# Optimization experiments

Hardware: AMD Instinct MI355X
Metric: run time of the kernel (lower is better)

Reference implementation:

```python
import jax, jax.numpy as jnp
import numpy as np
from jax import lax

N_QUBITS = 8
DEPTH = 2
IN_DIM = 512
LN_EPS = 1e-5


def _ry_shared(state, w, theta_w):
    # RY(theta) on wire w, shared angle across the batch. state: [B, 2,...,2]
    ax = w + 1
    c = jnp.cos(theta_w / 2)
    s = jnp.sin(theta_w / 2)
    s0 = lax.index_in_dim(state, 0, axis=ax, keepdims=True)
    s1 = lax.index_in_dim(state, 1, axis=ax, keepdims=True)
    return jnp.concatenate([c * s0 - s * s1, s * s0 + c * s1], axis=ax)


def _cnot(state, cw, tw):
    # CNOT control=cw, target=tw. state: [B, 2,...,2]
    ax_c = cw + 1
    ax_t = tw + 1
    s0 = lax.index_in_dim(state, 0, axis=ax_c, keepdims=True)
    s1 = lax.index_in_dim(state, 1, axis=ax_c, keepdims=True)
    s1 = jnp.flip(s1, axis=ax_t)
    return jnp.concatenate([s0, s1], axis=ax_c)


def _circuit(angles, theta):
    # angles: [B, n]; theta: [n]. Batched statevector sim (RY/CNOT are real).
    B, n = angles.shape
    half = angles * 0.5
    c = jnp.cos(half)
    s = jnp.sin(half)
    # Initial RY layer on |0...0> is a product state: qubit i -> [cos, sin]
    state = jnp.ones((B,), dtype=angles.dtype)
    for i in range(n):
        amp = jnp.stack([c[:, i], s[:, i]], axis=-1)  # [B, 2]
        state = state[..., None] * amp.reshape((B,) + (1,) * i + (2,))
    # state: [B, 2, 2, ..., 2] (n qubit axes)
    for _ in range(DEPTH):
        for i in range(n):
            state = _cnot(state, i, (i + 1) % n)
        for i in range(n):
            state = _ry_shared(state, i, theta[i])
    # <Z_i> = P(bit_i=0) - P(bit_i=1)
    p = state * state
    zs = []
    for i in range(n):
        axes = tuple(a for a in range(1, n + 1) if a != i + 1)
        m = p.sum(axis=axes)  # [B, 2]
        zs.append(m[:, 0] - m[:, 1])
    return jnp.stack(zs, axis=-1)  # [B, n]


def setup_inputs() -> dict:
    key = jax.random.key(0)
    ks = jax.random.split(key, 6)
    B = 131072
    return {
        "E": jax.random.normal(ks[0], (B, IN_DIM), dtype=jnp.float32),
        "ln_gamma": jnp.ones((IN_DIM,), dtype=jnp.float32),
        "ln_beta": jnp.zeros((IN_DIM,), dtype=jnp.float32),
        "W_pre": jax.random.normal(ks[1], (N_QUBITS, IN_DIM), dtype=jnp.float32) * (1.0 / np.sqrt(IN_DIM)),
        "b_pre": jax.random.normal(ks[2], (N_QUBITS,), dtype=jnp.float32) * 0.02,
        "theta": jax.random.normal(ks[3], (N_QUBITS,), dtype=jnp.float32) * 0.1,
        "W_post": jax.random.normal(ks[4], (1, N_QUBITS), dtype=jnp.float32) * (1.0 / np.sqrt(N_QUBITS)),
        "b_post": jax.random.normal(ks[5], (1,), dtype=jnp.float32) * 0.02,
    }


def reference(E, ln_gamma, ln_beta, W_pre, b_pre, theta, W_post, b_post):
    # pre: LayerNorm + Linear(in_dim -> n_qubits)
    mu = E.mean(axis=-1, keepdims=True)
    var = ((E - mu) ** 2).mean(axis=-1, keepdims=True)
    x = (E - mu) * lax.rsqrt(var + LN_EPS) * ln_gamma + ln_beta
    angles = x @ W_pre.T + b_pre  # [B, n_qubits]
    Z = _circuit(angles, theta)  # [B, n_qubits]
    logit_known = (Z @ W_post.T + b_post)[:, 0]  # squeeze(-1)
    return logit_known
```

## Files before the change

### kernel.cpp

```cpp
#include <hip/hip_runtime.h>

#define BLOCK 256
#define WPW   16

__device__ __forceinline__ float rfl(float x) {
  return __uint_as_float(__builtin_amdgcn_readfirstlane(__float_as_uint(x)));
}

template<int CTRL>
__device__ __forceinline__ float dppmov(float x) {
  return __int_as_float(__builtin_amdgcn_update_dpp(
      0, __float_as_int(x), CTRL, 0xf, 0xf, true));
}
__device__ __forceinline__ float dx1(float x) { return dppmov<0xB1>(x); }
__device__ __forceinline__ float dx2(float x) { return dppmov<0x4E>(x); }
__device__ __forceinline__ float dx4(float x) {
  return dppmov<0x1B>(dppmov<0x141>(x));
}
__device__ __forceinline__ float dx8(float x) { return dppmov<0x128>(x); }
__device__ __forceinline__ float sx16(float x) { return __shfl_xor(x, 16, 64); }
__device__ __forceinline__ float sx32(float x) { return __shfl_xor(x, 32, 64); }

template<int M>
__device__ __forceinline__ float lxor(float x) {
  if constexpr (M == 1)  return dx1(x);
  else if constexpr (M == 2)  return dx2(x);
  else if constexpr (M == 4)  return dx4(x);
  else if constexpr (M == 8)  return dx8(x);
  else if constexpr (M == 16) return sx16(x);
  else                        return sx32(x);
}

__device__ __forceinline__ float wave_allsum(float x) {
  x += dx1(x); x += dx2(x); x += dx4(x); x += dx8(x);
  x += sx16(x); x += sx32(x);
  return x;
}

__global__ __launch_bounds__(BLOCK, 4) void qsco_kernel(
    const float* __restrict__ E,
    const float* __restrict__ ln_gamma,
    const float* __restrict__ ln_beta,
    const float* __restrict__ Wpre,
    const float* __restrict__ bpre,
    const float* __restrict__ theta,
    const float* __restrict__ Wpost,
    const float* __restrict__ bpost,
    float* __restrict__ out,
    int nrows)
{
  const int lane = threadIdx.x & 63;
  const int wave = blockIdx.x * (BLOCK / 64) + (threadIdx.x >> 6);
  const int row0 = wave * WPW;
  if (row0 >= nrows) return;
  const int rowEnd = min(row0 + WPW, nrows);

  const int kA = lane << 2;
  const int kB = 256 + (lane << 2);

  const float4 gamA = *(const float4*)(ln_gamma + kA);
  const float4 gamB = *(const float4*)(ln_gamma + kB);
  const float4 betA = *(const float4*)(ln_beta + kA);
  const float4 betB = *(const float4*)(ln_beta + kB);

  float4 gv[8][2];
  float G[8], K[8];
#pragma unroll
  for (int j = 0; j < 8; ++j) {
    const float4 wA = *(const float4*)(Wpre + j * 512 + kA);
    const float4 wB = *(const float4*)(Wpre + j * 512 + kB);
    float4 ga, gb;
    ga.x = wA.x * gamA.x; ga.y = wA.y * gamA.y; ga.z = wA.z * gamA.z; ga.w = wA.w * gamA.w;
    gb.x = wB.x * gamB.x; gb.y = wB.y * gamB.y; gb.z = wB.z * gamB.z; gb.w = wB.w * gamB.w;
    gv[j][0] = ga; gv[j][1] = gb;
    float gs = (ga.x + ga.y + ga.z + ga.w) + (gb.x + gb.y + gb.z + gb.w);
    float ks = wA.x * betA.x + wA.y * betA.y + wA.z * betA.z + wA.w * betA.w
             + wB.x * betB.x + wB.y * betB.y + wB.z * betB.z + wB.w * betB.w;
    G[j] = rfl(wave_allsum(gs));
    K[j] = rfl(wave_allsum(ks) + bpre[j]);
  }

  float cT[8], sT[8];
#pragma unroll
  for (int q = 0; q < 8; ++q) {
    const float h = 0.5f * theta[q];
    cT[q] = rfl(__cosf(h));
    sT[q] = rfl(__sinf(h));
  }
  float ss[6];
#pragma unroll
  for (int q = 2; q < 8; ++q)
    ss[q - 2] = ((lane >> (q - 2)) & 1) ? sT[q] : -sT[q];

  float al[8];
#pragma unroll
  for (int q = 0; q < 8; ++q) al[q] = rfl(Wpost[q]);
  float base = 0.f;
#pragma unroll
  for (int q = 2; q < 8; ++q)
    base += ((lane >> (q - 2)) & 1) ? -al[q] : al[q];
  const float D0 = base + al[0] + al[1];
  const float D1 = base - al[0] + al[1];
  const float D2 = base + al[0] - al[1];
  const float D3 = base - al[0] - al[1];
  const float bp = rfl(bpost[0]);

  const float* Ep = E + (size_t)row0 * 512;
  float4 eA = *(const float4*)(Ep + kA);
  float4 eB = *(const float4*)(Ep + kB);

  for (int r = row0; r < rowEnd; ++r) {
    float4 nA = eA, nB = eB;
    if (r + 1 < rowEnd) {
      const float* En = E + (size_t)(r + 1) * 512;
      nA = *(const float4*)(En + kA);
      nB = *(const float4*)(En + kB);
    }

    float f[10];
    f[0] = (eA.x + eA.y + eA.z + eA.w) + (eB.x + eB.y + eB.z + eB.w);
    f[1] = eA.x * eA.x + eA.y * eA.y + eA.z * eA.z + eA.w * eA.w
         + eB.x * eB.x + eB.y * eB.y + eB.z * eB.z + eB.w * eB.w;
#pragma unroll
    for (int j = 0; j < 8; ++j) {
      const float4 ga = gv[j][0], gb = gv[j][1];
      f[2 + j] = eA.x * ga.x + eA.y * ga.y + eA.z * ga.z + eA.w * ga.w
               + eB.x * gb.x + eB.y * gb.y + eB.z * gb.z + eB.w * gb.w;
    }
#pragma unroll
    for (int i = 0; i < 10; ++i) f[i] += dx1(f[i]);
#pragma unroll
    for (int i = 0; i < 10; ++i) f[i] += dx2(f[i]);
#pragma unroll
    for (int i = 0; i < 10; ++i) f[i] += dx4(f[i]);
#pragma unroll
    for (int i = 0; i < 10; ++i) f[i] += dx8(f[i]);
#pragma unroll
    for (int i = 0; i < 10; ++i) f[i] += sx16(f[i]);
#pragma unroll
    for (int i = 0; i < 10; ++i) f[i] += sx32(f[i]);

    const float mu = f[0] * (1.0f / 512.0f);
    const float var = f[1] * (1.0f / 512.0f) - mu * mu;
    const float rstd = rsqrtf(var + 1e-5f);

    float ca[8], sa[8];
#pragma unroll
    for (int j = 0; j < 8; ++j) {
      const float ang = rstd * (f[2 + j] - mu * G[j]) + K[j];
      const float h = 0.5f * ang;
      ca[j] = __cosf(h);
      sa[j] = __sinf(h);
    }

    float p = ((lane & 1)  ? sa[2] : ca[2]);
    p      *= ((lane & 2)  ? sa[3] : ca[3]);
    p      *= ((lane & 4)  ? sa[4] : ca[4]);
    p      *= ((lane & 8)  ? sa[5] : ca[5]);
    p      *= ((lane & 16) ? sa[6] : ca[6]);
    p      *= ((lane & 32) ? sa[7] : ca[7]);
    const float pc = p * ca[1], ps = p * sa[1];
    float a0 = pc * ca[0], a1 = pc * sa[0], a2 = ps * ca[0], a3 = ps * sa[0];

#define CNOT_STEP(TM, CM) { \
      const float v0 = lxor<TM>(a0); \
      const float v1 = lxor<TM>(a1); \
      const float v2 = lxor<TM>(a2); \
      const float v3 = lxor<TM>(a3); \
      const bool c = (lane & (CM)) != 0; \
      a0 = c ? v0 : a0; a1 = c ? v1 : a1; a2 = c ? v2 : a2; a3 = c ? v3 : a3; }

#define RY_STEP(M, I) { \
      const float p0 = lxor<M>(a0); \
      const float p1 = lxor<M>(a1); \
      const float p2 = lxor<M>(a2); \
      const float p3 = lxor<M>(a3); \
      a0 = cT[(I) + 2] * a0 + ss[I] * p0; \
      a1 = cT[(I) + 2] * a1 + ss[I] * p1; \
      a2 = cT[(I) + 2] * a2 + ss[I] * p2; \
      a3 = cT[(I) + 2] * a3 + ss[I] * p3; }

#pragma unroll
    for (int d = 0; d < 2; ++d) {
      { const float t = a1; a1 = a3; a3 = t; }
      a2 = dx1(a2);
      a3 = dx1(a3);
      CNOT_STEP(2, 1)
      CNOT_STEP(4, 2)
      CNOT_STEP(8, 4)
      CNOT_STEP(16, 8)
      CNOT_STEP(32, 16)
      { const bool c = (lane & 32) != 0;
        const float t0 = c ? a1 : a0, t1 = c ? a0 : a1;
        const float t2 = c ? a3 : a2, t3 = c ? a2 : a3;
        a0 = t0; a1 = t1; a2 = t2; a3 = t3; }
      { float t = a0; a0 = cT[0] * t - sT[0] * a1; a1 = sT[0] * t + cT[0] * a1;
        t = a2;       a2 = cT[0] * t - sT[0] * a3; a3 = sT[0] * t + cT[0] * a3; }
      { float t = a0; a0 = cT[1] * t - sT[1] * a2; a2 = sT[1] * t + cT[1] * a2;
        t = a1;       a1 = cT[1] * t - sT[1] * a3; a3 = sT[1] * t + cT[1] * a3; }
      RY_STEP(1, 0)
      RY_STEP(2, 1)
      RY_STEP(4, 2)
      RY_STEP(8, 3)
      RY_STEP(16, 4)
      RY_STEP(32, 5)
    }
#undef CNOT_STEP
#undef RY_STEP

    float v = (a0 * a0) * D0 + (a1 * a1) * D1 + (a2 * a2) * D2 + (a3 * a3) * D3;
    v = wave_allsum(v);
    if (lane == 0) out[r] = v + bp;

    eA = nA; eB = nB;
  }
}

extern "C" void kernel_launch(void* const* d_in, const int* in_sizes, int n_in,
                              void* d_out, int out_size, void* d_ws, size_t ws_size,
                              hipStream_t stream) {
  const float* E        = (const float*)d_in[0];
  const float* ln_gamma = (const float*)d_in[1];
  const float* ln_beta  = (const float*)d_in[2];
  const float* Wpre     = (const float*)d_in[3];
  const float* bpre     = (const float*)d_in[4];
  const float* theta    = (const float*)d_in[5];
  const float* Wpost    = (const float*)d_in[6];
  const float* bpost    = (const float*)d_in[7];
  float* out = (float*)d_out;

  const int nrows = in_sizes[0] / 512;
  const int rows_per_block = (BLOCK / 64) * WPW;
  const int grid = (nrows + rows_per_block - 1) / rows_per_block;
  qsco_kernel<<<grid, BLOCK, 0, stream>>>(E, ln_gamma, ln_beta, Wpre, bpre,
                                          theta, Wpost, bpost, out, nrows);
}
```

Measured before the change: 397.2 us.

## Map 16 rows per wave with 4 lanes per row and register-held statevector

Result: slower. 405.5 us (+2.1%).

```diff
diff --git a/kernel.cpp b/kernel.cpp
--- a/kernel.cpp
+++ b/kernel.cpp
@@ -1,7 +1,6 @@
 #include <hip/hip_runtime.h>
 
 #define BLOCK 256
-#define WPW   16
 
 __device__ __forceinline__ float rfl(float x) {
   return __uint_as_float(__builtin_amdgcn_readfirstlane(__float_as_uint(x)));
@@ -21,21 +20,12 @@
 __device__ __forceinline__ float sx16(float x) { return __shfl_xor(x, 16, 64); }
 __device__ __forceinline__ float sx32(float x) { return __shfl_xor(x, 32, 64); }
 
-template<int M>
-__device__ __forceinline__ float lxor(float x) {
-  if constexpr (M == 1)  return dx1(x);
-  else if constexpr (M == 2)  return dx2(x);
-  else if constexpr (M == 4)  return dx4(x);
-  else if constexpr (M == 8)  return dx8(x);
-  else if constexpr (M == 16) return sx16(x);
-  else                        return sx32(x);
-}
-
 __device__ __forceinline__ float wave_allsum(float x) {
   x += dx1(x); x += dx2(x); x += dx4(x); x += dx8(x);
   x += sx16(x); x += sx32(x);
   return x;
 }
+
 
 __global__ __launch_bounds__(BLOCK, 4) void qsco_kernel(
     const float* __restrict__ E,
@@ -49,33 +39,37 @@
     float* __restrict__ out,
     int nrows)
 {
-  const int lane = threadIdx.x & 63;
-  const int wave = blockIdx.x * (BLOCK / 64) + (threadIdx.x >> 6);
-  const int row0 = wave * WPW;
-  if (row0 >= nrows) return;
-  const int rowEnd = min(row0 + WPW, nrows);
-
-  const int kA = lane << 2;
-  const int kB = 256 + (lane << 2);
-
-  const float4 gamA = *(const float4*)(ln_gamma + kA);
-  const float4 gamB = *(const float4*)(ln_gamma + kB);
-  const float4 betA = *(const float4*)(ln_beta + kA);
-  const float4 betB = *(const float4*)(ln_beta + kB);
-
-  float4 gv[8][2];
+  __shared__ float Wg[8][512];
+
+  const int tid  = threadIdx.x;
+  const int lane = tid & 63;
+
+#pragma unroll
+  for (int t = 0; t < 4; ++t) {
+    const int e4 = (t * BLOCK + tid) << 2;
+    const int j = e4 >> 9, k = e4 & 511;
+    const float4 w = *(const float4*)(Wpre + j * 512 + k);
+    const float4 g = *(const float4*)(ln_gamma + k);
+    float4 r;
+    r.x = w.x * g.x; r.y = w.y * g.y; r.z = w.z * g.z; r.w = w.w * g.w;
+    *(float4*)(&Wg[j][k]) = r;
+  }
+  __syncthreads();
+
+  const int k0 = lane << 3;
+  const float4 gamA = *(const float4*)(ln_gamma + k0);
+  const float4 gamB = *(const float4*)(ln_gamma + k0 + 4);
+  const float4 betA = *(const float4*)(ln_beta + k0);
+  const float4 betB = *(const float4*)(ln_beta + k0 + 4);
   float G[8], K[8];
 #pragma unroll
   for (int j = 0; j < 8; ++j) {
-    const float4 wA = *(const float4*)(Wpre + j * 512 + kA);
-    const float4 wB = *(const float4*)(Wpre + j * 512 + kB);
-    float4 ga, gb;
-    ga.x = wA.x * gamA.x; ga.y = wA.y * gamA.y; ga.z = wA.z * gamA.z; ga.w = wA.w * gamA.w;
-    gb.x = wB.x * gamB.x; gb.y = wB.y * gamB.y; gb.z = wB.z * gamB.z; gb.w = wB.w * gamB.w;
-    gv[j][0] = ga; gv[j][1] = gb;
-    float gs = (ga.x + ga.y + ga.z + ga.w) + (gb.x + gb.y + gb.z + gb.w);
-    float ks = wA.x * betA.x + wA.y * betA.y + wA.z * betA.z + wA.w * betA.w
-             + wB.x * betB.x + wB.y * betB.y + wB.z * betB.z + wB.w * betB.w;
+    const float4 wA = *(const float4*)(Wpre + j * 512 + k0);
+    const float4 wB = *(const float4*)(Wpre + j * 512 + k0 + 4);
+    const float gs = wA.x*gamA.x + wA.y*gamA.y + wA.z*gamA.z + wA.w*gamA.w
+                   + wB.x*gamB.x + wB.y*gamB.y + wB.z*gamB.z + wB.w*gamB.w;
+    const float ks = wA.x*betA.x + wA.y*betA.y + wA.z*betA.z + wA.w*betA.w
+                   + wB.x*betB.x + wB.y*betB.y + wB.z*betB.z + wB.w*betB.w;
     G[j] = rfl(wave_allsum(gs));
     K[j] = rfl(wave_allsum(ks) + bpre[j]);
   }
@@ -87,133 +81,154 @@
     cT[q] = rfl(__cosf(h));
     sT[q] = rfl(__sinf(h));
   }
-  float ss[6];
-#pragma unroll
-  for (int q = 2; q < 8; ++q)
-    ss[q - 2] = ((lane >> (q - 2)) & 1) ? sT[q] : -sT[q];
+  const float ss6 = (lane & 1) ? sT[6] : -sT[6];
+  const float ss7 = (lane & 2) ? sT[7] : -sT[7];
 
   float al[8];
 #pragma unroll
   for (int q = 0; q < 8; ++q) al[q] = rfl(Wpost[q]);
-  float base = 0.f;
-#pragma unroll
-  for (int q = 2; q < 8; ++q)
-    base += ((lane >> (q - 2)) & 1) ? -al[q] : al[q];
-  const float D0 = base + al[0] + al[1];
-  const float D1 = base - al[0] + al[1];
-  const float D2 = base + al[0] - al[1];
-  const float D3 = base - al[0] - al[1];
+  const float lsign = ((lane & 1) ? -al[6] : al[6]) + ((lane & 2) ? -al[7] : al[7]);
   const float bp = rfl(bpost[0]);
 
-  const float* Ep = E + (size_t)row0 * 512;
-  float4 eA = *(const float4*)(Ep + kA);
-  float4 eB = *(const float4*)(Ep + kB);
-
-  for (int r = row0; r < rowEnd; ++r) {
-    float4 nA = eA, nB = eB;
-    if (r + 1 < rowEnd) {
-      const float* En = E + (size_t)(r + 1) * 512;
-      nA = *(const float4*)(En + kA);
-      nB = *(const float4*)(En + kB);
-    }
-
-    float f[10];
-    f[0] = (eA.x + eA.y + eA.z + eA.w) + (eB.x + eB.y + eB.z + eB.w);
-    f[1] = eA.x * eA.x + eA.y * eA.y + eA.z * eA.z + eA.w * eA.w
-         + eB.x * eB.x + eB.y * eB.y + eB.z * eB.z + eB.w * eB.w;
+  const int wave = blockIdx.x * (BLOCK / 64) + (tid >> 6);
+  const int row  = wave * 16 + (lane >> 2);
+  const int sub  = lane & 3;
+  const float* Erow = E + (size_t)(row < nrows ? row : 0) * 512 + (sub << 2);
+
+  float f[10];
+#pragma unroll
+  for (int t = 0; t < 10; ++t) f[t] = 0.f;
+#pragma unroll 4
+  for (int i = 0; i < 32; ++i) {
+    const float4 ev = *(const float4*)(Erow + (i << 4));
+    const int kk = (sub << 2) + (i << 4);
+    f[0] += (ev.x + ev.y) + (ev.z + ev.w);
+    f[1] += ev.x*ev.x + ev.y*ev.y + ev.z*ev.z + ev.w*ev.w;
 #pragma unroll
     for (int j = 0; j < 8; ++j) {
-      const float4 ga = gv[j][0], gb = gv[j][1];
-      f[2 + j] = eA.x * ga.x + eA.y * ga.y + eA.z * ga.z + eA.w * ga.w
-               + eB.x * gb.x + eB.y * gb.y + eB.z * gb.z + eB.w * gb.w;
-    }
-#pragma unroll
-    for (int i = 0; i < 10; ++i) f[i] += dx1(f[i]);
-#pragma unroll
-    for (int i = 0; i < 10; ++i) f[i] += dx2(f[i]);
-#pragma unroll
-    for (int i = 0; i < 10; ++i) f[i] += dx4(f[i]);
-#pragma unroll
-    for (int i = 0; i < 10; ++i) f[i] += dx8(f[i]);
-#pragma unroll
-    for (int i = 0; i < 10; ++i) f[i] += sx16(f[i]);
-#pragma unroll
-    for (int i = 0; i < 10; ++i) f[i] += sx32(f[i]);
-
-    const float mu = f[0] * (1.0f / 512.0f);
-    const float var = f[1] * (1.0f / 512.0f) - mu * mu;
-    const float rstd = rsqrtf(var + 1e-5f);
-
-    float ca[8], sa[8];
-#pragma unroll
-    for (int j = 0; j < 8; ++j) {
-      const float ang = rstd * (f[2 + j] - mu * G[j]) + K[j];
-      const float h = 0.5f * ang;
-      ca[j] = __cosf(h);
-      sa[j] = __sinf(h);
-    }
-
-    float p = ((lane & 1)  ? sa[2] : ca[2]);
-    p      *= ((lane & 2)  ? sa[3] : ca[3]);
-    p      *= ((lane & 4)  ? sa[4] : ca[4]);
-    p      *= ((lane & 8)  ? sa[5] : ca[5]);
-    p      *= ((lane & 16) ? sa[6] : ca[6]);
-    p      *= ((lane & 32) ? sa[7] : ca[7]);
-    const float pc = p * ca[1], ps = p * sa[1];
-    float a0 = pc * ca[0], a1 = pc * sa[0], a2 = ps * ca[0], a3 = ps * sa[0];
-
-#define CNOT_STEP(TM, CM) { \
-      const float v0 = lxor<TM>(a0); \
-      const float v1 = lxor<TM>(a1); \
-      const float v2 = lxor<TM>(a2); \
-      const float v3 = lxor<TM>(a3); \
-      const bool c = (lane & (CM)) != 0; \
-      a0 = c ? v0 : a0; a1 = c ? v1 : a1; a2 = c ? v2 : a2; a3 = c ? v3 : a3; }
-
-#define RY_STEP(M, I) { \
-      const float p0 = lxor<M>(a0); \
-      const float p1 = lxor<M>(a1); \
-      const float p2 = lxor<M>(a2); \
-      const float p3 = lxor<M>(a3); \
-      a0 = cT[(I) + 2] * a0 + ss[I] * p0; \
-      a1 = cT[(I) + 2] * a1 + ss[I] * p1; \
-      a2 = cT[(I) + 2] * a2 + ss[I] * p2; \
-      a3 = cT[(I) + 2] * a3 + ss[I] * p3; }
-
-#pragma unroll
-    for (int d = 0; d < 2; ++d) {
-      { const float t = a1; a1 = a3; a3 = t; }
-      a2 = dx1(a2);
-      a3 = dx1(a3);
-      CNOT_STEP(2, 1)
-      CNOT_STEP(4, 2)
-      CNOT_STEP(8, 4)
-      CNOT_STEP(16, 8)
-      CNOT_STEP(32, 16)
-      { const bool c = (lane & 32) != 0;
-        const float t0 = c ? a1 : a0, t1 = c ? a0 : a1;
-        const float t2 = c ? a3 : a2, t3 = c ? a2 : a3;
-        a0 = t0; a1 = t1; a2 = t2; a3 = t3; }
-      { float t = a0; a0 = cT[0] * t - sT[0] * a1; a1 = sT[0] * t + cT[0] * a1;
-        t = a2;       a2 = cT[0] * t - sT[0] * a3; a3 = sT[0] * t + cT[0] * a3; }
-      { float t = a0; a0 = cT[1] * t - sT[1] * a2; a2 = sT[1] * t + cT[1] * a2;
-        t = a1;       a1 = cT[1] * t - sT[1] * a3; a3 = sT[1] * t + cT[1] * a3; }
-      RY_STEP(1, 0)
-      RY_STEP(2, 1)
-      RY_STEP(4, 2)
-      RY_STEP(8, 3)
-      RY_STEP(16, 4)
-      RY_STEP(32, 5)
-    }
-#undef CNOT_STEP
-#undef RY_STEP
-
-    float v = (a0 * a0) * D0 + (a1 * a1) * D1 + (a2 * a2) * D2 + (a3 * a3) * D3;
-    v = wave_allsum(v);
-    if (lane == 0) out[r] = v + bp;
-
-    eA = nA; eB = nB;
-  }
+      const float4 w = *(const float4*)(&Wg[j][kk]);
+      f[2 + j] += ev.x*w.x + ev.y*w.y + ev.z*w.z + ev.w*w.w;
+    }
+  }
+#pragma unroll
+  for (int t = 0; t < 10; ++t) f[t] += dx1(f[t]);
+#pragma unroll
+  for (int t = 0; t < 10; ++t) f[t] += dx2(f[t]);
+
+  const float mu   = f[0] * (1.0f / 512.0f);
+  const float var  = f[1] * (1.0f / 512.0f) - mu * mu;
+  const float rstd = rsqrtf(var + 1e-5f);
+
+  float ca[8], sa[8];
+#pragma unroll
+  for (int j = 0; j < 8; ++j) {
+    const float ang = rstd * (f[2 + j] - mu * G[j]) + K[j];
+    const float h = 0.5f * ang;
+    ca[j] = __cosf(h);
+    sa[j] = __sinf(h);
+  }
+
+  float a[64];
+  a[0] = ((lane & 1) ? sa[6] : ca[6]) * ((lane & 2) ? sa[7] : ca[7]);
+#pragma unroll
+  for (int b = 0; b < 6; ++b) {
+    const int m = 1 << b;
+#pragma unroll
+    for (int k = 0; k < 32; ++k) {
+      if (k < m) {
+        a[k + m] = a[k] * sa[b];
+        a[k]     = a[k] * ca[b];
+      }
+    }
+  }
+
+#pragma unroll
+  for (int d = 0; d < 2; ++d) {
+#pragma unroll
+    for (int k = 0; k < 64; ++k) if ((k & 1) && !(k & 2)) {
+      const float t_ = a[k]; a[k] = a[k ^ 2]; a[k ^ 2] = t_;
+    }
+#pragma unroll
+    for (int k = 0; k < 64; ++k) if ((k & 2) && !(k & 4)) {
+      const float t_ = a[k]; a[k] = a[k ^ 4]; a[k ^ 4] = t_;
+    }
+#pragma unroll
+    for (int k = 0; k < 64; ++k) if ((k & 4) && !(k & 8)) {
+      const float t_ = a[k]; a[k] = a[k ^ 8]; a[k ^ 8] = t_;
+    }
+#pragma unroll
+    for (int k = 0; k < 64; ++k) if ((k & 8) && !(k & 16)) {
+      const float t_ = a[k]; a[k] = a[k ^ 16]; a[k ^ 16] = t_;
+    }
+#pragma unroll
+    for (int k = 0; k < 64; ++k) if ((k & 16) && !(k & 32)) {
+      const float t_ = a[k]; a[k] = a[k ^ 32]; a[k ^ 32] = t_;
+    }
+#pragma unroll
+    for (int k = 32; k < 64; ++k) a[k] = dx1(a[k]);
+    {
+      const bool c = (lane & 1) != 0;
+#pragma unroll
+      for (int k = 0; k < 64; ++k) {
+        const float t_ = dx2(a[k]);
+        a[k] = c ? t_ : a[k];
+      }
+    }
+    {
+      const bool c = (lane & 2) != 0;
+#pragma unroll
+      for (int m = 0; m < 32; ++m) {
+        const float x = a[2 * m], y = a[2 * m + 1];
+        a[2 * m]     = c ? y : x;
+        a[2 * m + 1] = c ? x : y;
+      }
+    }
+#pragma unroll
+    for (int i = 0; i < 6; ++i) {
+      const int m = 1 << i;
+      const float cc = cT[i], sn = sT[i];
+#pragma unroll
+      for (int k = 0; k < 64; ++k) if (!(k & m)) {
+        const float x = a[k], y = a[k | m];
+        a[k]     = cc * x - sn * y;
+        a[k | m] = sn * x + cc * y;
+      }
+    }
+#pragma unroll
+    for (int k = 0; k < 64; ++k) {
+      const float p = dx1(a[k]);
+      a[k] = cT[6] * a[k] + ss6 * p;
+    }
+#pragma unroll
+    for (int k = 0; k < 64; ++k) {
+      const float p = dx2(a[k]);
+      a[k] = cT[7] * a[k] + ss7 * p;
+    }
+  }
+
+#pragma unroll
+  for (int k = 0; k < 64; ++k) a[k] = a[k] * a[k];
+  float zr[6];
+#pragma unroll
+  for (int b = 0; b < 6; ++b) {
+    const int n = 32 >> b;
+    float zb = 0.f;
+#pragma unroll
+    for (int m = 0; m < 32; ++m) {
+      if (m < n) {
+        const float p = a[2 * m], q = a[2 * m + 1];
+        zb   += (p - q);
+        a[m]  = p + q;
+      }
+    }
+    zr[b] = zb;
+  }
+  float vL = lsign * a[0];
+#pragma unroll
+  for (int i = 0; i < 6; ++i) vL += al[i] * zr[i];
+  vL += dx1(vL);
+  vL += dx2(vL);
+  if (sub == 0 && row < nrows) out[row] = vL + bp;
 }
 
 extern "C" void kernel_launch(void* const* d_in, const int* in_sizes, int n_in,
@@ -230,7 +245,7 @@
   float* out = (float*)d_out;
 
   const int nrows = in_sizes[0] / 512;
-  const int rows_per_block = (BLOCK / 64) * WPW;
+  const int rows_per_block = (BLOCK / 64) * 16;
   const int grid = (nrows + rows_per_block - 1) / rows_per_block;
   qsco_kernel<<<grid, BLOCK, 0, stream>>>(E, ln_gamma, ln_beta, Wpre, bpre,
                                           theta, Wpost, bpost, out, nrows);
```
